# Kernel optimization log

Measured on AMD Instinct MI355X. Metric: run time of the kernel, lower is better.

The kernel has to match this reference:

```python
import jax, jax.numpy as jnp
import numpy as np

NUM_HEADS = 4

def _proj(x, w, b):
    # Conv1d kernel_size=1 == pointwise linear over channels: [B, Cin, N] -> [B, Cout, N]
    return jnp.einsum('oi,bin->bon', w, x) + b[None, :, None]

def setup_inputs() -> dict:
    key = jax.random.key(0)
    ks = jax.random.split(key, 11)
    B, D, N = 8, 256, 2048
    inp = {
        'query': jax.random.normal(ks[0], (B, D, N), jnp.float32),
        'key':   jax.random.normal(ks[1], (B, D, N), jnp.float32),
        'value': jax.random.normal(ks[2], (B, D, N), jnp.float32),
        'w_q': jax.random.normal(ks[3], (D, D), jnp.float32) * (1.0 / np.sqrt(D)),
        'b_q': jax.random.normal(ks[4], (D,), jnp.float32) * 0.02,
        'w_k': jax.random.normal(ks[5], (D, D), jnp.float32) * (1.0 / np.sqrt(D)),
        'b_k': jax.random.normal(ks[6], (D,), jnp.float32) * 0.02,
        'w_v': jax.random.normal(ks[7], (D, D), jnp.float32) * (1.0 / np.sqrt(D)),
        'b_v': jax.random.normal(ks[8], (D,), jnp.float32) * 0.02,
        'w_m': jax.random.normal(ks[9], (D, D), jnp.float32) * (1.0 / np.sqrt(D)),
        'b_m': jax.random.normal(ks[10], (D,), jnp.float32) * 0.02,
    }
    return inp

def reference(query, key, value, w_q, b_q, w_k, b_k, w_v, b_v, w_m, b_m):
    B, D, N = query.shape
    H = NUM_HEADS
    d = D // H  # head dim (outer slot of channel split, matching torch .view)
    q = _proj(query, w_q, b_q).reshape(B, d, H, N)
    k = _proj(key,   w_k, b_k).reshape(B, d, H, N)
    v = _proj(value, w_v, b_v).reshape(B, d, H, N)
    scale = jnp.asarray(1.0 / np.sqrt(d), q.dtype)
    scores = jnp.einsum('bdhn,bdhm->bhnm', q, k) * scale  # [B,H,N,N]
    prob = jax.nn.softmax(scores, axis=-1)
    x = jnp.einsum('bhnm,bdhm->bdhn', prob, v)            # [B,d,H,N]
    out = _proj(x.reshape(B, D, N), w_m, b_m)             # [B,D,N]
    return out
```

## Files before the change

kernel.cpp:

```cpp
#include <hip/hip_runtime.h>
#include <cstdint>
#include <cstddef>

typedef unsigned short u16;
typedef unsigned int   u32;
typedef __attribute__((ext_vector_type(4))) float f32x4;
typedef __attribute__((ext_vector_type(16))) float f32x16;
typedef __attribute__((ext_vector_type(8))) short bf16x8;
typedef __attribute__((ext_vector_type(4))) unsigned short u16x4;
typedef __attribute__((ext_vector_type(2))) u32 u32x2;
typedef __attribute__((ext_vector_type(4))) u32 u32x4;

#define DEVI static __device__ __forceinline__
#define MFMA16(a,b,c) __builtin_amdgcn_mfma_f32_16x16x32_bf16((a),(b),(c),0,0,0)
#define MFMA32(a,b,c) __builtin_amdgcn_mfma_f32_32x32x16_bf16((a),(b),(c),0,0,0)
#define BAR()   __builtin_amdgcn_s_barrier()
#define CFENCE() asm volatile("" ::: "memory")

DEVI u16 f2b(float f) {
  u32 u = __builtin_bit_cast(u32, f);
  u32 r = u + 0x7fffu + ((u >> 16) & 1u);
  return (u16)(r >> 16);
}

DEVI u32 pkbf(float a, float b) {
  u32 r;
  asm("v_cvt_pk_bf16_f32 %0, %1, %2" : "=v"(r) : "v"(a), "v"(b));
  return r;
}

DEVI void load_lds16(const void* g, void* l) {
  __builtin_amdgcn_global_load_lds(
      (const __attribute__((address_space(1))) u32*)g,
      (__attribute__((address_space(3))) u32*)l, 16, 0, 0);
}

DEVI int perm_o(int o) { return 4 * (o & 63) + (o >> 6); }

__global__ __launch_bounds__(256) void k_prep_w(
    const float* __restrict__ wq, const float* __restrict__ wk,
    const float* __restrict__ wv, const float* __restrict__ wm,
    const float* __restrict__ bq, const float* __restrict__ bk, const float* __restrict__ bv,
    u16* __restrict__ WQ, u16* __restrict__ WK, u16* __restrict__ WV, u16* __restrict__ WM,
    float* __restrict__ BQ, float* __restrict__ BK, float* __restrict__ BV)
{
  int row = blockIdx.x, t = threadIdx.x, m = blockIdx.y;
  if (m == 0)      WQ[row * 256 + t] = f2b(wq[perm_o(row) * 256 + t]);
  else if (m == 1) WK[row * 256 + t] = f2b(wk[perm_o(row) * 256 + t]);
  else if (m == 2) WV[row * 256 + t] = f2b(wv[perm_o(row) * 256 + t]);
  else if (m == 3) WM[row * 256 + t] = f2b(wm[row * 256 + perm_o(t)]);
  else if (row == 0) {
    BQ[t] = bq[perm_o(t)];
    BK[t] = bk[perm_o(t)];
    BV[t] = bv[perm_o(t)];
  }
}

__global__ __launch_bounds__(256) void k_transpose(
    const float* __restrict__ q, const float* __restrict__ k, const float* __restrict__ v,
    u16* __restrict__ xq, u16* __restrict__ xk, u16* __restrict__ xv)
{
  __shared__ u16 tile[64][68];
  const int N = 2048, D = 256;
  int n0 = blockIdx.x * 64, c0 = blockIdx.y * 64;
  int b = blockIdx.z & 7, which = blockIdx.z >> 3;
  const float* src = (which == 0 ? q : which == 1 ? k : v) + (size_t)b * D * N;
  u16* dst = (which == 0 ? xq : which == 1 ? xk : xv) + (size_t)b * N * D;
  int t = threadIdx.x;
  int cl = t >> 4, ng = t & 15;
#pragma unroll
  for (int cc = 0; cc < 4; ++cc) {
    int c = cl + 16 * cc;
    f32x4 val = *(const f32x4*)&src[(size_t)(c0 + c) * N + n0 + ng * 4];
#pragma unroll
    for (int j = 0; j < 4; ++j) tile[c][ng * 4 + j] = f2b(val[j]);
  }
  __syncthreads();
  int n = t & 63, cq = t >> 6;
  union { u16 s[16]; u32x4 v4[2]; } pk;
#pragma unroll
  for (int j = 0; j < 16; ++j) pk.s[j] = tile[cq * 16 + j][n];
  u32x4* o = (u32x4*)&dst[(size_t)(n0 + n) * D + c0 + cq * 16];
  o[0] = pk.v4[0];
  o[1] = pk.v4[1];
}

template<int EPI>
__global__ __launch_bounds__(256, 4) void k_gemm(
    const u16* __restrict__ A, long sA,
    const u16* __restrict__ Bm, long sB,
    const float* __restrict__ bias,
    void* __restrict__ out, long sOut)
{
  __shared__ u16 lA[2][64 * 64];
  __shared__ u16 lB[2][64 * 64];
  int t = threadIdx.x, b = blockIdx.z;
  const u16* Ab = A + (size_t)b * sA + (size_t)blockIdx.x * 64 * 256;
  const u16* Bb = Bm + (size_t)b * sB + (size_t)blockIdx.y * 64 * 256;
  int l = t & 63, w = t >> 6, g = l >> 4, col = l & 15;
  int wr = w >> 1, wc = w & 1;
  f32x4 acc[2][2] = {};
  u32 sOf[2], sDs[2];
#pragma unroll
  for (int j = 0; j < 2; ++j) {
    int ci = t + 256 * j;
    int r = ci >> 3, c = ci & 7;
    sOf[j] = (u32)(r * 512 + ((c ^ (r & 7)) << 4));
    sDs[j] = (u32)(ci * 16);
  }
  auto stage = [&](int buf, int k0) {
#pragma unroll
    for (int j = 0; j < 2; ++j) {
      load_lds16((const char*)Ab + k0 * 2 + sOf[j], (char*)lA[buf] + sDs[j]);
      load_lds16((const char*)Bb + k0 * 2 + sOf[j], (char*)lB[buf] + sDs[j]);
    }
  };
  stage(0, 0);
  for (int s = 0; s < 4; ++s) {
    int cur = s & 1;
    if (s < 3) {
      stage(cur ^ 1, (s + 1) * 64);
      asm volatile("s_waitcnt vmcnt(4)" ::: "memory");
    } else {
      asm volatile("s_waitcnt vmcnt(0)" ::: "memory");
    }
    BAR(); CFENCE();
#pragma unroll
    for (int kc = 0; kc < 2; ++kc) {
      bf16x8 af[2], bfr[2];
#pragma unroll
      for (int mt = 0; mt < 2; ++mt) {
        int row = wr * 32 + mt * 16 + col;
        af[mt] = *(const bf16x8*)((const char*)lA[cur] + row * 128 + (((kc * 4 + g) ^ (row & 7)) << 4));
      }
#pragma unroll
      for (int nt = 0; nt < 2; ++nt) {
        int row = wc * 32 + nt * 16 + col;
        bfr[nt] = *(const bf16x8*)((const char*)lB[cur] + row * 128 + (((kc * 4 + g) ^ (row & 7)) << 4));
      }
#pragma unroll
      for (int mt = 0; mt < 2; ++mt)
#pragma unroll
        for (int nt = 0; nt < 2; ++nt)
          acc[mt][nt] = MFMA16(af[mt], bfr[nt], acc[mt][nt]);
    }
    if (s < 3) { CFENCE(); BAR(); }
  }
  if (EPI == 0) {
    u16* o = (u16*)out + (size_t)b * sOut;
#pragma unroll
    for (int nt = 0; nt < 2; ++nt) {
      int op = blockIdx.y * 64 + wc * 32 + nt * 16 + col;
      int hh = op >> 6, ii = op & 63;
      float bv = bias[op];
#pragma unroll
      for (int mt = 0; mt < 2; ++mt) {
        int nbase = blockIdx.x * 64 + wr * 32 + mt * 16 + g * 4;
#pragma unroll
        for (int r = 0; r < 4; ++r)
          o[((size_t)(hh * 2048 + nbase + r)) * 64 + ii] = f2b(acc[mt][nt][r] + bv);
      }
    }
  } else if (EPI == 1) {
    u16* o = (u16*)out + (size_t)b * sOut;
#pragma unroll
    for (int mt = 0; mt < 2; ++mt)
#pragma unroll
      for (int r = 0; r < 4; ++r) {
        int row = blockIdx.x * 64 + wr * 32 + mt * 16 + g * 4 + r;
        float bv = bias[row];
#pragma unroll
        for (int nt = 0; nt < 2; ++nt) {
          int cn = blockIdx.y * 64 + wc * 32 + nt * 16 + col;
          o[(size_t)row * 2048 + cn] = f2b(acc[mt][nt][r] + bv);
        }
      }
  } else {
    float* o = (float*)out + (size_t)b * sOut;
#pragma unroll
    for (int mt = 0; mt < 2; ++mt)
#pragma unroll
      for (int r = 0; r < 4; ++r) {
        int row = blockIdx.x * 64 + wr * 32 + mt * 16 + g * 4 + r;
        float bv = bias[row];
#pragma unroll
        for (int nt = 0; nt < 2; ++nt) {
          int cn = blockIdx.y * 64 + wc * 32 + nt * 16 + col;
          o[(size_t)row * 2048 + cn] = acc[mt][nt][r] + bv;
        }
      }
  }
}

__global__ __launch_bounds__(256, 2) void k_attn(
    const u16* __restrict__ Qt, const u16* __restrict__ Kt,
    const u16* __restrict__ Vw, u16* __restrict__ Xws)
{
  __shared__ u16 stg[4][2][4096];
  const float SC2 = 0.18033688011112042f;
  int t = threadIdx.x, l = t & 63;
  int w = t >> 6;
  int hi = l >> 5, col = l & 31;
  int lin = blockIdx.x;
  int xcd = lin & 7, j = lin >> 3;
  int bh = xcd * 4 + (j >> 4);
  int nb = j & 15;
  int b = bh >> 2, hh = bh & 3;
  const u16* Qb = Qt + ((size_t)(b * 4 + hh) * 2048) * 64;
  const u16* Kb = Kt + ((size_t)(b * 4 + hh) * 2048) * 64;
  const u16* Vb = Vw + ((size_t)(b * 256 + hh * 64)) * 2048;
  int nq = nb * 128 + w * 32 + col;

  bf16x8 qf[4];
#pragma unroll
  for (int ks = 0; ks < 4; ++ks)
    qf[ks] = *(const bf16x8*)&Qb[(size_t)nq * 64 + ks * 16 + hi * 8];

  u32 kSrc[2], vSrc[2], sDst[2];
#pragma unroll
  for (int jj = 0; jj < 2; ++jj) {
    int ci = t + 256 * jj;
    int r = ci >> 3, c = ci & 7;
    u32 sw = (u32)((c ^ ((r >> 1) & 7)) << 4);
    kSrc[jj] = (u32)(r * 128) + sw;
    vSrc[jj] = (u32)(r * 4096) + sw;
    sDst[jj] = (u32)(ci * 16);
  }
  u32 offC[4];
#pragma unroll
  for (int ks = 0; ks < 4; ++ks)
    offC[ks] = (u32)(((2 * ks + hi) ^ ((col >> 1) & 7)) << 4);

  bf16x8 ones;
  { union { u32 u[4]; bf16x8 v; } o; o.u[0] = o.u[1] = o.u[2] = o.u[3] = 0x3F803F80u; ones = o.v; }

  f32x16 xac0 = {}, xac1 = {}, xsum = {};
  float m_run = 0.0f;

  auto stage = [&](int buf, int tile) {
    const char* kb = (const char*)Kb + (size_t)tile * 8192;
    const char* vb = (const char*)Vb + (size_t)tile * 128;
#pragma unroll
    for (int jj = 0; jj < 2; ++jj)
      load_lds16(kb + kSrc[jj], (char*)stg[buf][0] + sDst[jj]);
#pragma unroll
    for (int jj = 0; jj < 2; ++jj)
      load_lds16(vb + vSrc[jj], (char*)stg[buf][1] + sDst[jj]);
  };

  stage(0, 0);
  stage(1, 1);
  for (int it = 0; it < 32; ++it) {
    int cur = it & 3;
    if (it < 30) {
      stage((it + 2) & 3, it + 2);
      if (__any(xsum[0] > 16777216.0f)) {
        const float ds = 5.9604644775390625e-8f;
        xac0 *= ds; xac1 *= ds; xsum *= ds;
        m_run += 24.0f;
      }
      asm volatile("s_waitcnt vmcnt(8)" ::: "memory");
    } else if (it == 30) {
      asm volatile("s_waitcnt vmcnt(4)" ::: "memory");
    } else {
      asm volatile("s_waitcnt vmcnt(0)" ::: "memory");
    }
    BAR(); CFENCE();
    const char* kK = (const char*)stg[cur][0] + col * 128;
    const char* kV = (const char*)stg[cur][1] + col * 128;

    f32x16 sac0 = {}, sac1 = {};
    __builtin_amdgcn_s_setprio(1);
#pragma unroll
    for (int ks = 0; ks < 4; ++ks) {
      bf16x8 kf0 = *(const bf16x8*)(kK + offC[ks]);
      bf16x8 kf1 = *(const bf16x8*)(kK + 4096 + offC[ks]);
      sac0 = MFMA32(kf0, qf[ks], sac0);
      sac1 = MFMA32(kf1, qf[ks], sac1);
    }
    __builtin_amdgcn_s_setprio(0);

    bf16x8 pf[4];
#pragma unroll
    for (int mt = 0; mt < 2; ++mt) {
      const f32x16& sc = mt ? sac1 : sac0;
      float p[16];
#pragma unroll
      for (int r = 0; r < 16; ++r)
        p[r] = __builtin_amdgcn_exp2f(__builtin_fmaf(sc[r], SC2, -m_run));
      u32 A0 = pkbf(p[0],  p[1]),  B0 = pkbf(p[2],  p[3]);
      u32 A1 = pkbf(p[4],  p[5]),  B1 = pkbf(p[6],  p[7]);
      u32 A2 = pkbf(p[8],  p[9]),  B2 = pkbf(p[10], p[11]);
      u32 A3 = pkbf(p[12], p[13]), B3 = pkbf(p[14], p[15]);
      asm("v_permlane32_swap_b32 %0, %1" : "+v"(A0), "+v"(A1));
      asm("v_permlane32_swap_b32 %0, %1" : "+v"(B0), "+v"(B1));
      asm("v_permlane32_swap_b32 %0, %1" : "+v"(A2), "+v"(A3));
      asm("v_permlane32_swap_b32 %0, %1" : "+v"(B2), "+v"(B3));
      union { u32 u[4]; bf16x8 v; } f0, f1;
      f0.u[0] = A0; f0.u[1] = B0; f0.u[2] = A1; f0.u[3] = B1;
      f1.u[0] = A2; f1.u[1] = B2; f1.u[2] = A3; f1.u[3] = B3;
      pf[mt * 2 + 0] = f0.v;
      pf[mt * 2 + 1] = f1.v;
    }

    __builtin_amdgcn_s_setprio(1);
#pragma unroll
    for (int S = 0; S < 4; ++S) {
      bf16x8 vf0 = *(const bf16x8*)(kV + offC[S]);
      bf16x8 vf1 = *(const bf16x8*)(kV + 4096 + offC[S]);
      xac0 = MFMA32(vf0, pf[S], xac0);
      xac1 = MFMA32(vf1, pf[S], xac1);
      xsum = MFMA32(ones, pf[S], xsum);
    }
    __builtin_amdgcn_s_setprio(0);
  }

  float inv = 1.0f / xsum[0];
  u16* Ob = Xws + (size_t)b * 2048 * 256 + (size_t)nq * 256 + hh * 64;
#pragma unroll
  for (int it2 = 0; it2 < 2; ++it2) {
    const f32x16& xa = it2 ? xac1 : xac0;
#pragma unroll
    for (int rq = 0; rq < 4; ++rq) {
      float v0 = xa[4 * rq + 0] * inv;
      float v1 = xa[4 * rq + 1] * inv;
      float v2 = xa[4 * rq + 2] * inv;
      float v3 = xa[4 * rq + 3] * inv;
      u32x2 w2; w2[0] = pkbf(v0, v1); w2[1] = pkbf(v2, v3);
      *(u32x2*)&Ob[it2 * 32 + 8 * rq + 4 * hi] = w2;
    }
  }
}

extern "C" void kernel_launch(void* const* d_in, const int* in_sizes, int n_in,
                              void* d_out, int out_size, void* d_ws, size_t ws_size,
                              hipStream_t stream)
{
  const float* q_in = (const float*)d_in[0];
  const float* k_in = (const float*)d_in[1];
  const float* v_in = (const float*)d_in[2];
  const float* w_q  = (const float*)d_in[3];
  const float* b_q  = (const float*)d_in[4];
  const float* w_k  = (const float*)d_in[5];
  const float* b_k  = (const float*)d_in[6];
  const float* w_v  = (const float*)d_in[7];
  const float* b_v  = (const float*)d_in[8];
  const float* w_m  = (const float*)d_in[9];
  const float* b_m  = (const float*)d_in[10];

  char* ws = (char*)d_ws;
  u16* XT_Q = (u16*)(ws + 0);
  u16* XT_K = (u16*)(ws + 8388608);
  u16* XT_V = (u16*)(ws + 16777216);
  u16* QT   = (u16*)(ws + 25165824);
  u16* KT   = (u16*)(ws + 33554432);
  u16* VW   = (u16*)(ws + 41943040);
  u16* WQ   = (u16*)(ws + 50331648);
  u16* WK   = (u16*)(ws + 50462720);
  u16* WV   = (u16*)(ws + 50593792);
  u16* WM   = (u16*)(ws + 50724864);
  float* BQ = (float*)(ws + 50855936);
  float* BK = (float*)(ws + 50856960);
  float* BV = (float*)(ws + 50857984);

  k_prep_w<<<dim3(256, 5), 256, 0, stream>>>(w_q, w_k, w_v, w_m, b_q, b_k, b_v,
                                             WQ, WK, WV, WM, BQ, BK, BV);
  k_transpose<<<dim3(32, 4, 24), 256, 0, stream>>>(q_in, k_in, v_in, XT_Q, XT_K, XT_V);
  k_gemm<0><<<dim3(32, 4, 8), 256, 0, stream>>>(XT_Q, 2048L * 256, WQ, 0, BQ, QT, 4L * 2048 * 64);
  k_gemm<0><<<dim3(32, 4, 8), 256, 0, stream>>>(XT_K, 2048L * 256, WK, 0, BK, KT, 4L * 2048 * 64);
  k_gemm<1><<<dim3(4, 32, 8), 256, 0, stream>>>(WV, 0, XT_V, 2048L * 256, BV, VW, 256L * 2048);
  k_attn<<<dim3(512), 256, 0, stream>>>(QT, KT, VW, XT_Q);
  k_gemm<2><<<dim3(4, 32, 8), 256, 0, stream>>>(WM, 0, XT_Q, 2048L * 256, b_m, d_out, 256L * 2048);
}
```

Baseline: 106.4 us.

## Merge prep kernels, batch QKV GEMMs, software-pipeline attention and drop rowsum MFMA

Merges weight prep and input transpose into one launch, and runs the Q, K and V projection GEMMs as a single launch with the epilogue chosen per block. In attention, the QK^T MFMAs for the next tile are issued before softmax and PV of the current tile, with a deeper stage lookahead. The softmax denominator is now summed from fp32 probabilities with a cross-half shuffle instead of an extra MFMA against a ones vector. This cuts launch count and MFMA work and overlaps compute phases, at the cost of higher register pressure from holding two score tiles.

```diff
diff --git a/kernel.cpp b/kernel.cpp
--- a/kernel.cpp
+++ b/kernel.cpp
@@ -7,7 +7,6 @@
 typedef __attribute__((ext_vector_type(4))) float f32x4;
 typedef __attribute__((ext_vector_type(16))) float f32x16;
 typedef __attribute__((ext_vector_type(8))) short bf16x8;
-typedef __attribute__((ext_vector_type(4))) unsigned short u16x4;
 typedef __attribute__((ext_vector_type(2))) u32 u32x2;
 typedef __attribute__((ext_vector_type(4))) u32 u32x4;
 
@@ -37,66 +36,85 @@
 
 DEVI int perm_o(int o) { return 4 * (o & 63) + (o >> 6); }
 
-__global__ __launch_bounds__(256) void k_prep_w(
+__global__ __launch_bounds__(256) void k_pre(
+    const float* __restrict__ q, const float* __restrict__ k, const float* __restrict__ v,
     const float* __restrict__ wq, const float* __restrict__ wk,
     const float* __restrict__ wv, const float* __restrict__ wm,
     const float* __restrict__ bq, const float* __restrict__ bk, const float* __restrict__ bv,
+    u16* __restrict__ xq, u16* __restrict__ xk, u16* __restrict__ xv,
     u16* __restrict__ WQ, u16* __restrict__ WK, u16* __restrict__ WV, u16* __restrict__ WM,
     float* __restrict__ BQ, float* __restrict__ BK, float* __restrict__ BV)
 {
-  int row = blockIdx.x, t = threadIdx.x, m = blockIdx.y;
-  if (m == 0)      WQ[row * 256 + t] = f2b(wq[perm_o(row) * 256 + t]);
-  else if (m == 1) WK[row * 256 + t] = f2b(wk[perm_o(row) * 256 + t]);
-  else if (m == 2) WV[row * 256 + t] = f2b(wv[perm_o(row) * 256 + t]);
-  else if (m == 3) WM[row * 256 + t] = f2b(wm[row * 256 + perm_o(t)]);
-  else if (row == 0) {
-    BQ[t] = bq[perm_o(t)];
-    BK[t] = bk[perm_o(t)];
-    BV[t] = bv[perm_o(t)];
-  }
-}
-
-__global__ __launch_bounds__(256) void k_transpose(
-    const float* __restrict__ q, const float* __restrict__ k, const float* __restrict__ v,
-    u16* __restrict__ xq, u16* __restrict__ xk, u16* __restrict__ xv)
-{
   __shared__ u16 tile[64][68];
-  const int N = 2048, D = 256;
-  int n0 = blockIdx.x * 64, c0 = blockIdx.y * 64;
-  int b = blockIdx.z & 7, which = blockIdx.z >> 3;
-  const float* src = (which == 0 ? q : which == 1 ? k : v) + (size_t)b * D * N;
-  u16* dst = (which == 0 ? xq : which == 1 ? xk : xv) + (size_t)b * N * D;
-  int t = threadIdx.x;
-  int cl = t >> 4, ng = t & 15;
-#pragma unroll
-  for (int cc = 0; cc < 4; ++cc) {
-    int c = cl + 16 * cc;
-    f32x4 val = *(const f32x4*)&src[(size_t)(c0 + c) * N + n0 + ng * 4];
-#pragma unroll
-    for (int j = 0; j < 4; ++j) tile[c][ng * 4 + j] = f2b(val[j]);
-  }
-  __syncthreads();
-  int n = t & 63, cq = t >> 6;
-  union { u16 s[16]; u32x4 v4[2]; } pk;
-#pragma unroll
-  for (int j = 0; j < 16; ++j) pk.s[j] = tile[cq * 16 + j][n];
-  u32x4* o = (u32x4*)&dst[(size_t)(n0 + n) * D + c0 + cq * 16];
-  o[0] = pk.v4[0];
-  o[1] = pk.v4[1];
-}
-
-template<int EPI>
-__global__ __launch_bounds__(256, 4) void k_gemm(
-    const u16* __restrict__ A, long sA,
-    const u16* __restrict__ Bm, long sB,
-    const float* __restrict__ bias,
-    void* __restrict__ out, long sOut)
+  int blk = blockIdx.x, t = threadIdx.x;
+  if (blk < 3072) {
+    const int N = 2048, D = 256;
+    int x = blk & 31, y = (blk >> 5) & 3, z = blk >> 7;
+    int n0 = x * 64, c0 = y * 64;
+    int b = z & 7, which = z >> 3;
+    const float* src = (which == 0 ? q : which == 1 ? k : v) + (size_t)b * D * N;
+    u16* dst = (which == 0 ? xq : which == 1 ? xk : xv) + (size_t)b * N * D;
+    int cl = t >> 4, ng = t & 15;
+#pragma unroll
+    for (int cc = 0; cc < 4; ++cc) {
+      int c = cl + 16 * cc;
+      f32x4 val = *(const f32x4*)&src[(size_t)(c0 + c) * N + n0 + ng * 4];
+#pragma unroll
+      for (int j = 0; j < 4; ++j) tile[c][ng * 4 + j] = f2b(val[j]);
+    }
+    __syncthreads();
+    int n = t & 63, cq = t >> 6;
+    union { u16 s[16]; u32x4 v4[2]; } pk;
+#pragma unroll
+    for (int j = 0; j < 16; ++j) pk.s[j] = tile[cq * 16 + j][n];
+    u32x4* o = (u32x4*)&dst[(size_t)(n0 + n) * D + c0 + cq * 16];
+    o[0] = pk.v4[0];
+    o[1] = pk.v4[1];
+  } else {
+    int p = blk - 3072;
+    int row = p & 255, m = p >> 8;
+    if (m == 0)      WQ[row * 256 + t] = f2b(wq[perm_o(row) * 256 + t]);
+    else if (m == 1) WK[row * 256 + t] = f2b(wk[perm_o(row) * 256 + t]);
+    else if (m == 2) WV[row * 256 + t] = f2b(wv[perm_o(row) * 256 + t]);
+    else if (m == 3) WM[row * 256 + t] = f2b(wm[row * 256 + perm_o(t)]);
+    else if (row == 0) {
+      BQ[t] = bq[perm_o(t)];
+      BK[t] = bk[perm_o(t)];
+      BV[t] = bv[perm_o(t)];
+    }
+  }
+}
+
+__global__ __launch_bounds__(256, 4) void k_gemm3(
+    const u16* __restrict__ XQ, const u16* __restrict__ XK, const u16* __restrict__ XV,
+    const u16* __restrict__ WQm, const u16* __restrict__ WKm, const u16* __restrict__ WVm,
+    const float* __restrict__ BQ, const float* __restrict__ BK, const float* __restrict__ BV,
+    u16* __restrict__ QT, u16* __restrict__ KT, u16* __restrict__ VW)
 {
   __shared__ u16 lA[2][64 * 64];
   __shared__ u16 lB[2][64 * 64];
-  int t = threadIdx.x, b = blockIdx.z;
-  const u16* Ab = A + (size_t)b * sA + (size_t)blockIdx.x * 64 * 256;
-  const u16* Bb = Bm + (size_t)b * sB + (size_t)blockIdx.y * 64 * 256;
+  int gid = blockIdx.x, t = threadIdx.x;
+  int wk = gid >> 10, rem = gid & 1023;
+  int b = rem >> 7;
+  int bx, by, epi;
+  const u16 *Ab, *Bb;
+  const float* bias;
+  u16* outp;
+  if (wk < 2) {
+    bx = rem & 31; by = (rem >> 5) & 3;
+    Ab = (wk ? XK : XQ) + (size_t)b * (2048 * 256) + (size_t)bx * 64 * 256;
+    Bb = (wk ? WKm : WQm) + (size_t)by * 64 * 256;
+    bias = wk ? BK : BQ;
+    outp = (wk ? KT : QT) + (size_t)b * (4L * 2048 * 64);
+    epi = 0;
+  } else {
+    bx = rem & 3; by = (rem >> 2) & 31;
+    Ab = WVm + (size_t)bx * 64 * 256;
+    Bb = XV + (size_t)b * (2048 * 256) + (size_t)by * 64 * 256;
+    bias = BV;
+    outp = VW + (size_t)b * (256L * 2048);
+    epi = 1;
+  }
   int l = t & 63, w = t >> 6, g = l >> 4, col = l & 15;
   int wr = w >> 1, wc = w & 1;
   f32x4 acc[2][2] = {};
@@ -146,50 +164,109 @@
     }
     if (s < 3) { CFENCE(); BAR(); }
   }
-  if (EPI == 0) {
-    u16* o = (u16*)out + (size_t)b * sOut;
+  if (epi == 0) {
 #pragma unroll
     for (int nt = 0; nt < 2; ++nt) {
-      int op = blockIdx.y * 64 + wc * 32 + nt * 16 + col;
+      int op = by * 64 + wc * 32 + nt * 16 + col;
       int hh = op >> 6, ii = op & 63;
       float bv = bias[op];
 #pragma unroll
       for (int mt = 0; mt < 2; ++mt) {
-        int nbase = blockIdx.x * 64 + wr * 32 + mt * 16 + g * 4;
+        int nbase = bx * 64 + wr * 32 + mt * 16 + g * 4;
 #pragma unroll
         for (int r = 0; r < 4; ++r)
-          o[((size_t)(hh * 2048 + nbase + r)) * 64 + ii] = f2b(acc[mt][nt][r] + bv);
-      }
-    }
-  } else if (EPI == 1) {
-    u16* o = (u16*)out + (size_t)b * sOut;
+          outp[((size_t)(hh * 2048 + nbase + r)) * 64 + ii] = f2b(acc[mt][nt][r] + bv);
+      }
+    }
+  } else {
 #pragma unroll
     for (int mt = 0; mt < 2; ++mt)
 #pragma unroll
       for (int r = 0; r < 4; ++r) {
-        int row = blockIdx.x * 64 + wr * 32 + mt * 16 + g * 4 + r;
+        int row = bx * 64 + wr * 32 + mt * 16 + g * 4 + r;
         float bv = bias[row];
 #pragma unroll
         for (int nt = 0; nt < 2; ++nt) {
-          int cn = blockIdx.y * 64 + wc * 32 + nt * 16 + col;
-          o[(size_t)row * 2048 + cn] = f2b(acc[mt][nt][r] + bv);
+          int cn = by * 64 + wc * 32 + nt * 16 + col;
+          outp[(size_t)row * 2048 + cn] = f2b(acc[mt][nt][r] + bv);
         }
       }
-  } else {
-    float* o = (float*)out + (size_t)b * sOut;
-#pragma unroll
-    for (int mt = 0; mt < 2; ++mt)
-#pragma unroll
-      for (int r = 0; r < 4; ++r) {
-        int row = blockIdx.x * 64 + wr * 32 + mt * 16 + g * 4 + r;
-        float bv = bias[row];
-#pragma unroll
-        for (int nt = 0; nt < 2; ++nt) {
-          int cn = blockIdx.y * 64 + wc * 32 + nt * 16 + col;
-          o[(size_t)row * 2048 + cn] = acc[mt][nt][r] + bv;
-        }
-      }
-  }
+  }
+}
+
+__global__ __launch_bounds__(256, 4) void k_gemmM(
+    const u16* __restrict__ A,
+    const u16* __restrict__ Bm, long sB,
+    const float* __restrict__ bias,
+    float* __restrict__ out, long sOut)
+{
+  __shared__ u16 lA[2][64 * 64];
+  __shared__ u16 lB[2][64 * 64];
+  int t = threadIdx.x, b = blockIdx.z;
+  const u16* Ab = A + (size_t)blockIdx.x * 64 * 256;
+  const u16* Bb = Bm + (size_t)b * sB + (size_t)blockIdx.y * 64 * 256;
+  int l = t & 63, w = t >> 6, g = l >> 4, col = l & 15;
+  int wr = w >> 1, wc = w & 1;
+  f32x4 acc[2][2] = {};
+  u32 sOf[2], sDs[2];
+#pragma unroll
+  for (int j = 0; j < 2; ++j) {
+    int ci = t + 256 * j;
+    int r = ci >> 3, c = ci & 7;
+    sOf[j] = (u32)(r * 512 + ((c ^ (r & 7)) << 4));
+    sDs[j] = (u32)(ci * 16);
+  }
+  auto stage = [&](int buf, int k0) {
+#pragma unroll
+    for (int j = 0; j < 2; ++j) {
+      load_lds16((const char*)Ab + k0 * 2 + sOf[j], (char*)lA[buf] + sDs[j]);
+      load_lds16((const char*)Bb + k0 * 2 + sOf[j], (char*)lB[buf] + sDs[j]);
+    }
+  };
+  stage(0, 0);
+  for (int s = 0; s < 4; ++s) {
+    int cur = s & 1;
+    if (s < 3) {
+      stage(cur ^ 1, (s + 1) * 64);
+      asm volatile("s_waitcnt vmcnt(4)" ::: "memory");
+    } else {
+      asm volatile("s_waitcnt vmcnt(0)" ::: "memory");
+    }
+    BAR(); CFENCE();
+#pragma unroll
+    for (int kc = 0; kc < 2; ++kc) {
+      bf16x8 af[2], bfr[2];
+#pragma unroll
+      for (int mt = 0; mt < 2; ++mt) {
+        int row = wr * 32 + mt * 16 + col;
+        af[mt] = *(const bf16x8*)((const char*)lA[cur] + row * 128 + (((kc * 4 + g) ^ (row & 7)) << 4));
+      }
+#pragma unroll
+      for (int nt = 0; nt < 2; ++nt) {
+        int row = wc * 32 + nt * 16 + col;
+        bfr[nt] = *(const bf16x8*)((const char*)lB[cur] + row * 128 + (((kc * 4 + g) ^ (row & 7)) << 4));
+      }
+#pragma unroll
+      for (int mt = 0; mt < 2; ++mt)
+#pragma unroll
+        for (int nt = 0; nt < 2; ++nt)
+          acc[mt][nt] = MFMA16(af[mt], bfr[nt], acc[mt][nt]);
+    }
+    if (s < 3) { CFENCE(); BAR(); }
+  }
+  float* o = out + (size_t)b * sOut;
+#pragma unroll
+  for (int mt = 0; mt < 2; ++mt)
+#pragma unroll
+    for (int r = 0; r < 4; ++r) {
+      int row = blockIdx.x * 64 + wr * 32 + mt * 16 + g * 4 + r;
+      float bv = bias[row];
+#pragma unroll
+      for (int nt = 0; nt < 2; ++nt) {
+        int cn = blockIdx.y * 64 + wc * 32 + nt * 16 + col;
+        o[(size_t)row * 2048 + cn] = acc[mt][nt][r] + bv;
+      }
+    }
 }
 
 __global__ __launch_bounds__(256, 2) void k_attn(
@@ -230,12 +307,10 @@
 #pragma unroll
   for (int ks = 0; ks < 4; ++ks)
     offC[ks] = (u32)(((2 * ks + hi) ^ ((col >> 1) & 7)) << 4);
-
-  bf16x8 ones;
-  { union { u32 u[4]; bf16x8 v; } o; o.u[0] = o.u[1] = o.u[2] = o.u[3] = 0x3F803F80u; ones = o.v; }
-
-  f32x16 xac0 = {}, xac1 = {}, xsum = {};
-  float m_run = 0.0f;
+  u32 colb = (u32)(col * 128);
+
+  f32x16 xac0 = {}, xac1 = {};
+  float psum = 0.0f, m_run = 0.0f;
 
   auto stage = [&](int buf, int tile) {
     const char* kb = (const char*)Kb + (size_t)tile * 8192;
@@ -248,46 +323,31 @@
       load_lds16(vb + vSrc[jj], (char*)stg[buf][1] + sDst[jj]);
   };
 
-  stage(0, 0);
-  stage(1, 1);
-  for (int it = 0; it < 32; ++it) {
-    int cur = it & 3;
-    if (it < 30) {
-      stage((it + 2) & 3, it + 2);
-      if (__any(xsum[0] > 16777216.0f)) {
-        const float ds = 5.9604644775390625e-8f;
-        xac0 *= ds; xac1 *= ds; xsum *= ds;
-        m_run += 24.0f;
-      }
-      asm volatile("s_waitcnt vmcnt(8)" ::: "memory");
-    } else if (it == 30) {
-      asm volatile("s_waitcnt vmcnt(4)" ::: "memory");
-    } else {
-      asm volatile("s_waitcnt vmcnt(0)" ::: "memory");
-    }
-    BAR(); CFENCE();
-    const char* kK = (const char*)stg[cur][0] + col * 128;
-    const char* kV = (const char*)stg[cur][1] + col * 128;
-
-    f32x16 sac0 = {}, sac1 = {};
+  auto do_qk = [&](int buf, f32x16& s0, f32x16& s1) {
+    const char* kK = (const char*)stg[buf][0] + colb;
     __builtin_amdgcn_s_setprio(1);
 #pragma unroll
     for (int ks = 0; ks < 4; ++ks) {
       bf16x8 kf0 = *(const bf16x8*)(kK + offC[ks]);
       bf16x8 kf1 = *(const bf16x8*)(kK + 4096 + offC[ks]);
-      sac0 = MFMA32(kf0, qf[ks], sac0);
-      sac1 = MFMA32(kf1, qf[ks], sac1);
+      s0 = MFMA32(kf0, qf[ks], s0);
+      s1 = MFMA32(kf1, qf[ks], s1);
     }
     __builtin_amdgcn_s_setprio(0);
-
+  };
+
+  auto do_sm_pv = [&](int buf, const f32x16& s0, const f32x16& s1) {
     bf16x8 pf[4];
+    float ps = 0.0f;
 #pragma unroll
     for (int mt = 0; mt < 2; ++mt) {
-      const f32x16& sc = mt ? sac1 : sac0;
+      const f32x16& sc = mt ? s1 : s0;
       float p[16];
 #pragma unroll
-      for (int r = 0; r < 16; ++r)
+      for (int r = 0; r < 16; ++r) {
         p[r] = __builtin_amdgcn_exp2f(__builtin_fmaf(sc[r], SC2, -m_run));
+        ps += p[r];
+      }
       u32 A0 = pkbf(p[0],  p[1]),  B0 = pkbf(p[2],  p[3]);
       u32 A1 = pkbf(p[4],  p[5]),  B1 = pkbf(p[6],  p[7]);
       u32 A2 = pkbf(p[8],  p[9]),  B2 = pkbf(p[10], p[11]);
@@ -302,7 +362,8 @@
       pf[mt * 2 + 0] = f0.v;
       pf[mt * 2 + 1] = f1.v;
     }
-
+    psum += ps;
+    const char* kV = (const char*)stg[buf][1] + colb;
     __builtin_amdgcn_s_setprio(1);
 #pragma unroll
     for (int S = 0; S < 4; ++S) {
@@ -310,12 +371,45 @@
       bf16x8 vf1 = *(const bf16x8*)(kV + 4096 + offC[S]);
       xac0 = MFMA32(vf0, pf[S], xac0);
       xac1 = MFMA32(vf1, pf[S], xac1);
-      xsum = MFMA32(ones, pf[S], xsum);
     }
     __builtin_amdgcn_s_setprio(0);
-  }
-
-  float inv = 1.0f / xsum[0];
+  };
+
+  stage(0, 0);
+  stage(1, 1);
+  asm volatile("s_waitcnt vmcnt(4)" ::: "memory");
+  BAR(); CFENCE();
+  f32x16 sA0 = {}, sA1 = {};
+  do_qk(0, sA0, sA1);
+  stage(2, 2);
+
+  for (int it = 0; it < 31; ++it) {
+    if (__any(psum > 16777216.0f)) {
+      const float ds = 5.9604644775390625e-8f;
+      xac0 *= ds; xac1 *= ds; psum *= ds;
+      m_run += 24.0f;
+    }
+    if (it < 30) {
+      asm volatile("s_waitcnt vmcnt(4)" ::: "memory");
+    } else {
+      asm volatile("s_waitcnt vmcnt(0)" ::: "memory");
+    }
+    BAR(); CFENCE();
+    if (it + 3 <= 31) stage((it + 3) & 3, it + 3);
+    f32x16 sB0 = {}, sB1 = {};
+    do_qk((it + 1) & 3, sB0, sB1);
+    do_sm_pv(it & 3, sA0, sA1);
+    sA0 = sB0; sA1 = sB1;
+  }
+  if (__any(psum > 16777216.0f)) {
+    const float ds = 5.9604644775390625e-8f;
+    xac0 *= ds; xac1 *= ds; psum *= ds;
+    m_run += 24.0f;
+  }
+  do_sm_pv(31 & 3, sA0, sA1);
+
+  psum += __shfl_xor(psum, 32);
+  float inv = 1.0f / psum;
   u16* Ob = Xws + (size_t)b * 2048 * 256 + (size_t)nq * 256 + hh * 64;
 #pragma unroll
   for (int it2 = 0; it2 < 2; ++it2) {
@@ -363,12 +457,12 @@
   float* BK = (float*)(ws + 50856960);
   float* BV = (float*)(ws + 50857984);
 
-  k_prep_w<<<dim3(256, 5), 256, 0, stream>>>(w_q, w_k, w_v, w_m, b_q, b_k, b_v,
-                                             WQ, WK, WV, WM, BQ, BK, BV);
-  k_transpose<<<dim3(32, 4, 24), 256, 0, stream>>>(q_in, k_in, v_in, XT_Q, XT_K, XT_V);
-  k_gemm<0><<<dim3(32, 4, 8), 256, 0, stream>>>(XT_Q, 2048L * 256, WQ, 0, BQ, QT, 4L * 2048 * 64);
-  k_gemm<0><<<dim3(32, 4, 8), 256, 0, stream>>>(XT_K, 2048L * 256, WK, 0, BK, KT, 4L * 2048 * 64);
-  k_gemm<1><<<dim3(4, 32, 8), 256, 0, stream>>>(WV, 0, XT_V, 2048L * 256, BV, VW, 256L * 2048);
+  k_pre<<<dim3(4352), 256, 0, stream>>>(q_in, k_in, v_in, w_q, w_k, w_v, w_m,
+                                        b_q, b_k, b_v, XT_Q, XT_K, XT_V,
+                                        WQ, WK, WV, WM, BQ, BK, BV);
+  k_gemm3<<<dim3(3072), 256, 0, stream>>>(XT_Q, XT_K, XT_V, WQ, WK, WV,
+                                          BQ, BK, BV, QT, KT, VW);
   k_attn<<<dim3(512), 256, 0, stream>>>(QT, KT, VW, XT_Q);
-  k_gemm<2><<<dim3(4, 32, 8), 256, 0, stream>>>(WM, 0, XT_Q, 2048L * 256, b_m, d_out, 256L * 2048);
-}
+  k_gemmM<<<dim3(4, 32, 8), 256, 0, stream>>>(WM, XT_Q, 2048L * 256, b_m,
+                                              (float*)d_out, 256L * 2048);
+}
```

New measurement: 99.76 us. 6.2% less time.
